# Kernel optimization log

Measured on AMD Instinct MI355X. Metric: run time of the kernel, lower is better.

## Reference

```python
import math
import jax, jax.numpy as jnp
import numpy as np

CHUNK = 32
EPS = 1e-5


def l2norm(x):
    return x * jax.lax.rsqrt(jnp.sum(x * x, -1, keepdims=True))


def causal_dwconv(x, w):
    # x: (B, C, L); w: (C, K) depthwise causal conv (left pad K-1)
    C, K = w.shape
    return jax.lax.conv_general_dilated(x, w[:, None, :], (1,), [(K - 1, 0)], feature_group_count=C)


def per_head_stats(x):
    # x: (B,L,H,D) -> (B,L,H,4): mean, var(pop), abs-mean, l2-norm
    mean = jnp.mean(x, -1, keepdims=True)
    var = jnp.mean(x * x, -1, keepdims=True) - mean * mean
    abs_mean = jnp.mean(jnp.abs(x), -1, keepdims=True)
    l2 = jnp.sqrt(jnp.sum(x * x, -1, keepdims=True))
    return jnp.concatenate([mean, var, abs_mean, l2], -1)


def delta_rule_chunkwise(q, k, v, beta, chunk=CHUNK):
    # q,k: (B,H,L,dk); v: (B,H,L,dv); beta: (B,H,L)
    b, h, L, dk = q.shape
    dv = v.shape[-1]
    pad = (-L) % chunk
    if pad:
        pc = ((0, 0), (0, 0), (0, pad), (0, 0))
        q, k, v = (jnp.pad(t, pc) for t in (q, k, v))
        beta = jnp.pad(beta, ((0, 0), (0, 0), (0, pad)))
    Lp = L + pad
    n = Lp // chunk
    q = l2norm(q)
    k = l2norm(k)
    v = v * beta[..., None]
    kb = k * beta[..., None]
    resh = lambda t: t.reshape(b, h, n, chunk, t.shape[-1])
    q, k, v, kb = map(resh, (q, k, v, kb))
    tri = jnp.triu(jnp.ones((chunk, chunk), bool))          # incl. diag
    strict = jnp.triu(jnp.ones((chunk, chunk), bool), 1)    # above diag
    A = jnp.where(tri, 0.0, -jnp.einsum('bhncd,bhned->bhnce', kb, k))
    # forward-substitution inverse of (I - strict_lower) as in the torch loop
    for i in range(1, chunk):
        upd = jnp.einsum('...k,...kj->...j', A[..., i, :], A[..., :, :i])
        A = A.at[..., i, :i].add(upd)
    inv = A + jnp.eye(chunk, dtype=A.dtype)
    u = inv @ v   # (b,h,n,c,dv)
    w = inv @ kb  # (b,h,n,c,dk)

    def step(S, xs):
        qi, ki, ui, wi = xs  # (b,h,c,d)
        attn = jnp.where(strict, 0.0, qi @ jnp.swapaxes(ki, -1, -2))
        u_adj = ui - wi @ S
        out_i = qi @ S + attn @ u_adj
        S = S + jnp.swapaxes(ki, -1, -2) @ u_adj
        return S, out_i

    xs = tuple(jnp.moveaxis(t, 2, 0) for t in (q, k, u, w))
    S0 = jnp.zeros((b, h, dk, dv), q.dtype)
    S, outs = jax.lax.scan(step, S0, xs)
    out = jnp.moveaxis(outs, 0, 2).reshape(b, h, Lp, dv)[:, :, :L]
    return out, S


def reference(hidden_states, q_proj_w, k_proj_w, v_proj_w, b_proj_w,
              q_conv_w, k_conv_w, v_conv_w, fir_short_w, fir_long_w,
              fuse_w1, fuse_b1, fuse_w2, fuse_b2, logit_temp,
              res_scale_short, res_scale_long, o_norm_w, o_proj_w):
    B, L, D = hidden_states.shape
    H = fir_short_w.shape[0]

    def shortconv(x, w):  # x: (B,L,C)
        y = causal_dwconv(jnp.swapaxes(x, 1, 2), w)
        return jax.nn.silu(jnp.swapaxes(y, 1, 2))

    q = shortconv(hidden_states @ q_proj_w.T, q_conv_w)
    k = shortconv(hidden_states @ k_proj_w.T, k_conv_w)
    v = shortconv(hidden_states @ v_proj_w.T, v_conv_w)
    q = q.reshape(B, L, H, -1)
    k = k.reshape(B, L, H, -1)
    v_direct = v.reshape(B, L, H, -1)
    beta = jax.nn.sigmoid(hidden_states @ b_proj_w.T)  # (B,L,H)

    delta_out, _S = delta_rule_chunkwise(
        jnp.transpose(q, (0, 2, 1, 3)), jnp.transpose(k, (0, 2, 1, 3)),
        jnp.transpose(v_direct, (0, 2, 1, 3)), jnp.transpose(beta, (0, 2, 1)))
    delta_out = jnp.transpose(delta_out, (0, 2, 1, 3))

    def fir(x, filt):  # x: (B,L,H,Dh); filt: (H,Dh,K)
        hh, dd, kk = filt.shape
        xf = jnp.swapaxes(x.reshape(B, L, hh * dd), 1, 2)
        y = causal_dwconv(xf, filt.reshape(hh * dd, kk))
        return jnp.swapaxes(y, 1, 2).reshape(B, L, hh, dd)

    local_short = fir(v_direct, fir_short_w)
    local_long = fir(v_direct, fir_long_w)

    stats = jnp.concatenate([per_head_stats(t) for t in
                             (local_short, local_long, delta_out, v_direct)], -1)  # (B,L,H,16)
    hs_exp = jnp.broadcast_to(hidden_states[:, :, None, :], (B, L, H, D))
    gate_in = jnp.concatenate([hs_exp, stats], -1)
    hdn = jax.nn.gelu(gate_in @ fuse_w1.T + fuse_b1, approximate=False)
    logits = hdn @ fuse_w2.T + fuse_b2  # (B,L,H,4)
    temp = jax.nn.softplus(logit_temp) + 1e-4
    fw = jax.nn.softmax(logits / temp, -1)

    o = (fw[..., 0:1] * local_short + fw[..., 1:2] * local_long
         + fw[..., 2:3] * delta_out + fw[..., 3:4] * v_direct)
    o = o + res_scale_short * local_short + res_scale_long * local_long
    o = o * jax.lax.rsqrt(jnp.mean(o * o, -1, keepdims=True) + EPS) * o_norm_w
    return o.reshape(B, L, -1) @ o_proj_w.T


def setup_inputs() -> dict:
    key = jax.random.key(0)
    ks = jax.random.split(key, 16)
    B, L, D, H = 2, 4096, 1024, 4
    dk, dv = D, D
    dh = dv // H
    gate_in_dim = D + 16
    gate_hidden = D * 2 // 2
    s = 0.02
    f32 = jnp.float32
    return {
        'hidden_states': jax.random.normal(ks[0], (B, L, D), f32),
        'q_proj_w': jax.random.normal(ks[1], (dk, D), f32) * s,
        'k_proj_w': jax.random.normal(ks[2], (dk, D), f32) * s,
        'v_proj_w': jax.random.normal(ks[3], (dv, D), f32) * s,
        'b_proj_w': jax.random.normal(ks[4], (H, D), f32) * s,
        'q_conv_w': jax.random.normal(ks[5], (dk, 4), f32) * 0.1,
        'k_conv_w': jax.random.normal(ks[6], (dk, 4), f32) * 0.1,
        'v_conv_w': jax.random.normal(ks[7], (dv, 4), f32) * 0.1,
        'fir_short_w': jax.random.normal(ks[8], (H, dh, 5), f32) * 0.02,
        'fir_long_w': jax.random.normal(ks[9], (H, dh, 64), f32) * 0.02,
        'fuse_w1': jax.random.normal(ks[10], (gate_hidden, gate_in_dim), f32) * s,
        'fuse_b1': jnp.zeros((gate_hidden,), f32),
        'fuse_w2': jax.random.normal(ks[11], (4, gate_hidden), f32) * s,
        'fuse_b2': jnp.array([-1.0, -1.0, 1.0, 3.0], f32),
        'logit_temp': jnp.full((1,), math.log(math.expm1(0.7)), f32),
        'res_scale_short': jnp.full((1,), 0.1, f32),
        'res_scale_long': jnp.full((1,), 0.1, f32),
        'o_norm_w': jnp.ones((dh,), f32),
        'o_proj_w': jax.random.normal(ks[12], (D, dv), f32) * s,
    }
```

## Files before the change

kernel.cpp:

```cpp
#include <hip/hip_runtime.h>
#include <hip/hip_bf16.h>

#define BB 2
#define LL 4096
#define DD 1024
#define HH 4
#define DH 256
#define CH 32
#define NC (LL/CH)
#define BL (BB*LL)
#define BLD ((size_t)BB*LL*DD)

typedef __attribute__((ext_vector_type(8))) short short8;
typedef __attribute__((ext_vector_type(4))) float floatx4;

__device__ __forceinline__ float bf2f(unsigned short u) {
    union { float f; unsigned int i; } x; x.i = ((unsigned int)u) << 16; return x.f;
}
__device__ __forceinline__ float bflo(unsigned int u) {
    union { float f; unsigned int i; } x; x.i = u << 16; return x.f;
}
__device__ __forceinline__ float bfhi(unsigned int u) {
    union { float f; unsigned int i; } x; x.i = u & 0xFFFF0000u; return x.f;
}
__device__ __forceinline__ unsigned short f2bf(float f) {
    union { float f; unsigned int i; } x; x.f = f;
    unsigned int r = x.i + 0x7FFFu + ((x.i >> 16) & 1u);
    return (unsigned short)(r >> 16);
}
__device__ __forceinline__ unsigned int pkbf(float a, float b) {
    unsigned int ua = __float_as_uint(a) + 0x8000u;
    unsigned int ub = __float_as_uint(b) + 0x8000u;
    return __builtin_amdgcn_perm(ub, ua, 0x07060302);
}
__device__ __forceinline__ void lds_barrier() {
    __builtin_amdgcn_s_waitcnt(0xC07F);
    __builtin_amdgcn_s_barrier();
}
__device__ __forceinline__ short8 gload16(const void* p) {
    short8 r;
    asm volatile("global_load_dwordx4 %0, %1, off" : "=v"(r) : "v"(p) : "memory");
    return r;
}
__device__ __forceinline__ uint2 gload8(const void* p) {
    uint2 r;
    asm volatile("global_load_dwordx2 %0, %1, off" : "=v"(r) : "v"(p) : "memory");
    return r;
}

__global__ __launch_bounds__(256) void cvt_bf_k(
    const float* __restrict__ x, unsigned short* __restrict__ y)
{
    size_t i = ((size_t)blockIdx.x * 256 + threadIdx.x) * 4;
    float4 v = *(const float4*)(x + i);
    ushort4 o;
    o.x = f2bf(v.x); o.y = f2bf(v.y); o.z = f2bf(v.z); o.w = f2bf(v.w);
    *(ushort4*)(y + i) = o;
}

__global__ __launch_bounds__(256) void w1s_prep_k(
    const float* __restrict__ w1, unsigned short* __restrict__ w1s)
{
    int idx = blockIdx.x * 256 + threadIdx.x;
    int e = idx >> 4, s = idx & 15;
    w1s[idx] = f2bf(w1[(size_t)e * 1040 + 1024 + s]);
}

__global__ __launch_bounds__(256) void gemm_mfma(
    const float* __restrict__ A, int lda,
    const float* __restrict__ W, int ldw,
    const float* __restrict__ bias,
    float* __restrict__ C, int ldc, int K)
{
    __shared__ unsigned short Abuf[128][56];
    __shared__ unsigned short Bbuf[128][56];
    const int t = threadIdx.x;
    const int wave = t >> 6, lane = t & 63;
    const int wm = wave >> 1, wn = wave & 1;
    const int row0 = blockIdx.y * 128, col0 = blockIdx.x * 128;

    floatx4 acc[4][4];
#pragma unroll
    for (int i = 0; i < 4; ++i)
#pragma unroll
        for (int j = 0; j < 4; ++j) acc[i][j] = (floatx4){0.f, 0.f, 0.f, 0.f};

    const int fr = lane & 15, fk = (lane >> 4) * 8;

    for (int kt = 0; kt < K; kt += 32) {
        __syncthreads();
#pragma unroll
        for (int it = 0; it < 2; ++it) {
            int idx = t + it * 256;
            int r = idx >> 2, s = (idx & 3) * 8;
            const float* ap = A + (size_t)(row0 + r) * lda + kt + s;
            float4 a0 = *(const float4*)(ap);
            float4 a1 = *(const float4*)(ap + 4);
            ushort4 p0, p1;
            p0.x = f2bf(a0.x); p0.y = f2bf(a0.y); p0.z = f2bf(a0.z); p0.w = f2bf(a0.w);
            p1.x = f2bf(a1.x); p1.y = f2bf(a1.y); p1.z = f2bf(a1.z); p1.w = f2bf(a1.w);
            *(ushort4*)&Abuf[r][s]     = p0;
            *(ushort4*)&Abuf[r][s + 4] = p1;
            const float* wp = W + (size_t)(col0 + r) * ldw + kt + s;
            float4 b0 = *(const float4*)(wp);
            float4 b1 = *(const float4*)(wp + 4);
            ushort4 q0, q1;
            q0.x = f2bf(b0.x); q0.y = f2bf(b0.y); q0.z = f2bf(b0.z); q0.w = f2bf(b0.w);
            q1.x = f2bf(b1.x); q1.y = f2bf(b1.y); q1.z = f2bf(b1.z); q1.w = f2bf(b1.w);
            *(ushort4*)&Bbuf[r][s]     = q0;
            *(ushort4*)&Bbuf[r][s + 4] = q1;
        }
        __syncthreads();

        short8 afrag[4], bfrag[4];
#pragma unroll
        for (int i = 0; i < 4; ++i) {
            afrag[i] = *(const short8*)&Abuf[wm * 64 + i * 16 + fr][fk];
            bfrag[i] = *(const short8*)&Bbuf[wn * 64 + i * 16 + fr][fk];
        }
#pragma unroll
        for (int i = 0; i < 4; ++i)
#pragma unroll
            for (int j = 0; j < 4; ++j)
                acc[i][j] = __builtin_amdgcn_mfma_f32_16x16x32_bf16(
                    afrag[i], bfrag[j], acc[i][j], 0, 0, 0);
    }

    const int fc = lane & 15, frow = (lane >> 4) * 4;
#pragma unroll
    for (int j = 0; j < 4; ++j) {
        int col = col0 + wn * 64 + j * 16 + fc;
        float bv = bias ? bias[col] : 0.0f;
#pragma unroll
        for (int i = 0; i < 4; ++i) {
#pragma unroll
            for (int r = 0; r < 4; ++r) {
                int row = row0 + wm * 64 + i * 16 + frow + r;
                C[(size_t)row * ldc + col] = acc[i][j][r] + bv;
            }
        }
    }
}

__global__ __launch_bounds__(256) void gemm_bb(
    const unsigned short* __restrict__ A, int lda,
    const unsigned short* __restrict__ B, int ldb,
    float* __restrict__ C, int ldc, int K)
{
    __shared__ unsigned short Abuf[128][56];
    __shared__ unsigned short Bbuf[128][56];
    const int t = threadIdx.x;
    const int wave = t >> 6, lane = t & 63;
    const int wm = wave >> 1, wn = wave & 1;
    const int row0 = blockIdx.y * 128, col0 = blockIdx.x * 128;

    floatx4 acc[4][4];
#pragma unroll
    for (int i = 0; i < 4; ++i)
#pragma unroll
        for (int j = 0; j < 4; ++j) acc[i][j] = (floatx4){0.f, 0.f, 0.f, 0.f};

    const int fr = lane & 15, fk = (lane >> 4) * 8;

    for (int kt = 0; kt < K; kt += 32) {
        __syncthreads();
#pragma unroll
        for (int it = 0; it < 2; ++it) {
            int idx = t + it * 256;
            int r = idx >> 2, s = (idx & 3) * 8;
            uint4 av = *(const uint4*)(A + (size_t)(row0 + r) * lda + kt + s);
            *(uint4*)&Abuf[r][s] = av;
            uint4 bv = *(const uint4*)(B + (size_t)(col0 + r) * ldb + kt + s);
            *(uint4*)&Bbuf[r][s] = bv;
        }
        __syncthreads();

        short8 afrag[4], bfrag[4];
#pragma unroll
        for (int i = 0; i < 4; ++i) {
            afrag[i] = *(const short8*)&Abuf[wm * 64 + i * 16 + fr][fk];
            bfrag[i] = *(const short8*)&Bbuf[wn * 64 + i * 16 + fr][fk];
        }
#pragma unroll
        for (int i = 0; i < 4; ++i)
#pragma unroll
            for (int j = 0; j < 4; ++j)
                acc[i][j] = __builtin_amdgcn_mfma_f32_16x16x32_bf16(
                    afrag[i], bfrag[j], acc[i][j], 0, 0, 0);
    }

    const int fc = lane & 15, frow = (lane >> 4) * 4;
#pragma unroll
    for (int j = 0; j < 4; ++j) {
        int col = col0 + wn * 64 + j * 16 + fc;
#pragma unroll
        for (int i = 0; i < 4; ++i) {
#pragma unroll
            for (int r = 0; r < 4; ++r) {
                int row = row0 + wm * 64 + i * 16 + frow + r;
                C[(size_t)row * ldc + col] = acc[i][j][r];
            }
        }
    }
}

__global__ __launch_bounds__(256) void convnorm_qk_k(
    const float* __restrict__ x, const float* __restrict__ w,
    unsigned short* __restrict__ y)
{
    int bl = blockIdx.x >> 2;
    int h  = blockIdx.x & 3;
    int l  = bl & (LL - 1);
    int d  = threadIdx.x;
    int c  = h * DH + d;
    const float* wp = w + (size_t)c * 4;
    const float* xp = x + (size_t)bl * DD + c;
    float acc = wp[3] * xp[0];
    if (l >= 1) acc += wp[2] * xp[-(int)DD];
    if (l >= 2) acc += wp[1] * xp[-2*(int)DD];
    if (l >= 3) acc += wp[0] * xp[-3*(int)DD];
    acc = acc / (1.0f + expf(-acc));
    float s = acc * acc;
#pragma unroll
    for (int off = 32; off > 0; off >>= 1) s += __shfl_down(s, off);
    __shared__ float red[4];
    int wv = threadIdx.x >> 6, ln = threadIdx.x & 63;
    if (ln == 0) red[wv] = s;
    __syncthreads();
    float tot = red[0] + red[1] + red[2] + red[3];
    y[(size_t)bl * DD + c] = f2bf(acc * rsqrtf(tot));
}

__global__ __launch_bounds__(256) void conv_silu_k(
    const float* __restrict__ x, const float* __restrict__ w, float* __restrict__ y)
{
    size_t idx = (size_t)blockIdx.x * 256 + threadIdx.x;
    int c = (int)(idx & (DD - 1));
    int bl = (int)(idx >> 10);
    int l = bl & (LL - 1);
    const float* wp = w + (size_t)c * 4;
    const float* xp = x + (size_t)bl * DD + c;
    float acc = wp[3] * xp[0];
    if (l >= 1) acc += wp[2] * xp[-(int)DD];
    if (l >= 2) acc += wp[1] * xp[-2*(int)DD];
    if (l >= 3) acc += wp[0] * xp[-3*(int)DD];
    y[idx] = acc / (1.0f + expf(-acc));
}

template<int K>
__global__ __launch_bounds__(256) void fir2_k(
    const float* __restrict__ x, const float* __restrict__ filt, float* __restrict__ y)
{
    const int ctile = blockIdx.x & 15;
    const int ltile = (blockIdx.x >> 4) & 63;
    const int b = blockIdx.x >> 10;
    const int RT = 64 + K - 1;
    __shared__ float xs[RT][64];
    __shared__ float fs[64][K + 1];
    const int t = threadIdx.x;
    const int l0 = ltile * 64;

    for (int i = t; i < RT * 16; i += 256) {
        int li = i >> 4, c4 = (i & 15) * 4;
        int l = l0 - (K - 1) + li;
        float4 v = make_float4(0.f, 0.f, 0.f, 0.f);
        if (l >= 0)
            v = *(const float4*)(x + ((size_t)b * LL + l) * DD + ctile * 64 + c4);
        *(float4*)&xs[li][c4] = v;
    }
    for (int i = t; i < 64 * K; i += 256) {
        fs[i / K][i % K] = filt[(size_t)ctile * 64 * K + i];
    }
    __syncthreads();

    const int c = t & 63, lg = t >> 6;
    float acc[16];
#pragma unroll
    for (int o = 0; o < 16; ++o) acc[o] = 0.f;
#pragma unroll
    for (int j = 0; j < 16 + K - 1; ++j) {
        float xv = xs[lg * 16 + j][c];
#pragma unroll
        for (int o = 0; o < 16; ++o) {
            int tap = j - o;
            if (tap >= 0 && tap < K) acc[o] += fs[c][tap] * xv;
        }
    }
    size_t base = ((size_t)b * LL + l0 + lg * 16) * DD + ctile * 64 + c;
#pragma unroll
    for (int o = 0; o < 16; ++o)
        y[base + (size_t)o * DD] = acc[o];
}

__global__ __launch_bounds__(256) void beta_k(
    const float* __restrict__ hs, const float* __restrict__ bw, float* __restrict__ beta)
{
    int bl = blockIdx.x;
    const float* xr = hs + (size_t)bl * DD;
    float a0=0.f,a1=0.f,a2=0.f,a3=0.f;
    for (int k = threadIdx.x; k < DD; k += 256) {
        float xv = xr[k];
        a0 += xv * bw[k];
        a1 += xv * bw[DD + k];
        a2 += xv * bw[2*DD + k];
        a3 += xv * bw[3*DD + k];
    }
#pragma unroll
    for (int off = 32; off > 0; off >>= 1) {
        a0 += __shfl_down(a0, off); a1 += __shfl_down(a1, off);
        a2 += __shfl_down(a2, off); a3 += __shfl_down(a3, off);
    }
    __shared__ float red[4][4];
    int wv = threadIdx.x >> 6, ln = threadIdx.x & 63;
    if (ln == 0) { red[wv][0]=a0; red[wv][1]=a1; red[wv][2]=a2; red[wv][3]=a3; }
    __syncthreads();
    if (threadIdx.x < 4) {
        int h = threadIdx.x;
        float s = red[0][h] + red[1][h] + red[2][h] + red[3][h];
        beta[(size_t)bl * HH + h] = 1.0f / (1.0f + expf(-s));
    }
}

__global__ __launch_bounds__(256) void tr_k(
    const unsigned short* __restrict__ k, unsigned short* __restrict__ kT)
{
    int et = blockIdx.x & 3;
    int lt = (blockIdx.x >> 2) & 63;
    int bh = blockIdx.x >> 8;
    int h = bh & 3, b = bh >> 2;
    __shared__ unsigned short tile[64][72];
    int t = threadIdx.x;
    int tr = t >> 4;
    int tc = (t & 15) * 4;
#pragma unroll
    for (int i = 0; i < 4; ++i) {
        int l = tr + i * 16;
        ushort4 v = *(const ushort4*)(k + ((size_t)b * LL + lt*64 + l) * DD + h * DH + et*64 + tc);
        *(ushort4*)&tile[l][tc] = v;
    }
    __syncthreads();
#pragma unroll
    for (int i = 0; i < 4; ++i) {
        int e = tr + i * 16;
        ushort4 v;
        v.x = tile[tc+0][e]; v.y = tile[tc+1][e];
        v.z = tile[tc+2][e]; v.w = tile[tc+3][e];
        *(ushort4*)(kT + ((size_t)bh * DH + et*64 + e) * LL + (size_t)lt*64 + tc) = v;
    }
}

__global__ __launch_bounds__(256) void chunk_prep2_k(
    const unsigned short* __restrict__ q, const unsigned short* __restrict__ k,
    const unsigned short* __restrict__ kT, const float* __restrict__ v,
    const float* __restrict__ beta,
    unsigned short* __restrict__ uT, unsigned short* __restrict__ w_out,
    unsigned short* __restrict__ attn_out)
{
    const int ci = blockIdx.x & (NC - 1);
    const int bh = blockIdx.x >> 7;
    const int h = bh & (HH - 1), b = bh >> 2;
    __shared__ unsigned short kL[32][264];
    __shared__ unsigned short qL[32][264];
    __shared__ float vL[32][260];
    __shared__ float AmL[32][33];
    __shared__ unsigned short AbH[32][40];
    __shared__ unsigned short AbL2[32][40];
    __shared__ float betL[32];
    const int t = threadIdx.x;
    const int wave = t >> 6, lane = t & 63;
    const int lr = lane & 15, lg = lane >> 4;
    const int l0 = ci * CH;
    const size_t rowbase = (size_t)b * LL + l0;

    for (int i = t; i < 1024; i += 256) {
        int r = i >> 5, s8 = (i & 31) * 8;
        *(uint4*)&kL[r][s8] = *(const uint4*)(k + (rowbase + r) * DD + h * DH + s8);
        *(uint4*)&qL[r][s8] = *(const uint4*)(q + (rowbase + r) * DD + h * DH + s8);
    }
    for (int i = t; i < 2048; i += 256) {
        int e = i >> 6, d4 = (i & 63) * 4;
        *(float4*)&vL[e][d4] = *(const float4*)(v + (rowbase + e) * DD + h * DH + d4);
    }
    if (t < 32) betL[t] = beta[(rowbase + t) * HH + h];
    __syncthreads();

    const int mt = wave >> 1, nt = wave & 1;
    floatx4 accA = (floatx4){0.f,0.f,0.f,0.f}, accT = accA;
#pragma unroll
    for (int ks = 0; ks < 8; ++ks) {
        short8 bk = *(const short8*)&kL[nt * 16 + lr][ks * 32 + lg * 8];
        short8 ak = *(const short8*)&kL[mt * 16 + lr][ks * 32 + lg * 8];
        short8 aq = *(const short8*)&qL[mt * 16 + lr][ks * 32 + lg * 8];
        accA = __builtin_amdgcn_mfma_f32_16x16x32_bf16(ak, bk, accA, 0, 0, 0);
        accT = __builtin_amdgcn_mfma_f32_16x16x32_bf16(aq, bk, accT, 0, 0, 0);
    }
    {
        const size_t abase = (size_t)blockIdx.x * (CH * CH);
        const int ee = nt * 16 + lr;
#pragma unroll
        for (int r = 0; r < 4; ++r) {
            int c = mt * 16 + lg * 4 + r;
            float bc = betL[c];
            AmL[c][ee] = (ee < c) ? (-bc * accA[r]) : 0.0f;
            attn_out[abase + (size_t)c * CH + ee] =
                (ee <= c) ? f2bf(accT[r]) : (unsigned short)0;
        }
    }
    __syncthreads();

    const unsigned short* kTg = kT + (size_t)bh * DH * LL;
    short8 wB[4];
#pragma unroll
    for (int n = 0; n < 4; ++n)
        wB[n] = *(const short8*)(kTg + (size_t)(wave * 64 + n * 16 + lr) * LL + l0 + lg * 8);

    if (wave == 0) {
        const int j = lane & 31;
        float col[32];
#pragma unroll
        for (int c = 0; c < 32; ++c) col[c] = AmL[c][j];
#pragma unroll
        for (int i = 1; i < 32; ++i) {
            float u0 = 0.f, u1 = 0.f;
#pragma unroll
            for (int kk = 0; kk < 32; kk += 2) {
                if (kk < i)     u0 += __shfl(col[i], kk) * col[kk];
                if (kk + 1 < i) u1 += __shfl(col[i], kk + 1) * col[kk + 1];
            }
            if (j < i) col[i] += u0 + u1;
        }
        if (lane < 32) {
            const float bj = betL[j];
#pragma unroll
            for (int c = 0; c < 32; ++c) {
                float val = (col[c] + (c == j ? 1.0f : 0.0f)) * bj;
                unsigned short hi = f2bf(val);
                AbH[c][j] = hi;
                AbL2[c][j] = f2bf(val - bf2f(hi));
            }
        }
    }
    __syncthreads();

    short8 AH[2], ALo[2];
#pragma unroll
    for (int m = 0; m < 2; ++m) {
        AH[m]  = *(const short8*)&AbH[m * 16 + lr][lg * 8];
        ALo[m] = *(const short8*)&AbL2[m * 16 + lr][lg * 8];
    }
    const size_t uTbase = (size_t)bh * DH * LL;
    const size_t wbase  = (size_t)bh * LL * DH;
#pragma unroll
    for (int n = 0; n < 4; ++n) {
        const int d = wave * 64 + n * 16 + lr;
        union { short8 s8; unsigned int u[4]; } vf;
#pragma unroll
        for (int p2 = 0; p2 < 4; ++p2)
            vf.u[p2] = pkbf(vL[lg * 8 + p2 * 2][d], vL[lg * 8 + p2 * 2 + 1][d]);
#pragma unroll
        for (int m = 0; m < 2; ++m) {
            floatx4 au = (floatx4){0.f,0.f,0.f,0.f};
            au = __builtin_amdgcn_mfma_f32_16x16x32_bf16(AH[m],  vf.s8, au, 0, 0, 0);
            au = __builtin_amdgcn_mfma_f32_16x16x32_bf16(ALo[m], vf.s8, au, 0, 0, 0);
            ushort4 ou;
            ou.x = f2bf(au[0]); ou.y = f2bf(au[1]); ou.z = f2bf(au[2]); ou.w = f2bf(au[3]);
            *(ushort4*)(uT + uTbase + (size_t)d * LL + l0 + m * 16 + lg * 4) = ou;

            floatx4 aw = (floatx4){0.f,0.f,0.f,0.f};
            aw = __builtin_amdgcn_mfma_f32_16x16x32_bf16(AH[m],  wB[n], aw, 0, 0, 0);
            aw = __builtin_amdgcn_mfma_f32_16x16x32_bf16(ALo[m], wB[n], aw, 0, 0, 0);
#pragma unroll
            for (int r = 0; r < 4; ++r)
                w_out[wbase + (size_t)(l0 + m * 16 + lg * 4 + r) * DH + d] = f2bf(aw[r]);
        }
    }
}

__global__ __launch_bounds__(256, 1) void scan12_k(
    const unsigned short* __restrict__ q, const unsigned short* __restrict__ kT,
    const unsigned short* __restrict__ uT, const unsigned short* __restrict__ w,
    const unsigned short* __restrict__ attn, float* __restrict__ dout)
{
    const int bh = blockIdx.x & 7;
    const int jb = blockIdx.x >> 3;
    const int h = bh & (HH - 1), b = bh >> 2;
    const int jcol = jb * 16;
    const int wave = threadIdx.x >> 6, lane = threadIdx.x & 63;
    const int lr = lane & 15, lg = lane >> 4;
    const int half = wave & 1;
    const bool isQ = wave >= 2;

    __shared__ unsigned short SbT[16][264];
    __shared__ unsigned short uadjT[16][40];

    floatx4 Sacc[4];
#pragma unroll
    for (int mt = 0; mt < 4; ++mt) Sacc[mt] = (floatx4){0.f,0.f,0.f,0.f};

    const unsigned short* qb  = q + (size_t)b * LL * DD + h * DH;
    const unsigned short* wb  = w + (size_t)bh * LL * DH;
    const unsigned short* ob  = isQ ? qb : wb;
    const size_t ost          = isQ ? (size_t)DD : (size_t)DH;
    const unsigned short* orow0 = ob + (size_t)(half * 16 + lr) * ost + lg * 8;
    const unsigned short* kTb = kT + (size_t)bh * DH * LL
                                + (size_t)(64 * wave + lr) * LL + lg * 8;
    const unsigned short* uTb = uT + ((size_t)bh * DH + jcol + lr) * LL + half * 16 + lg * 4;
    const unsigned short* atb = attn + (size_t)bh * NC * (CH * CH)
                                + (size_t)(half * 16 + lr) * CH + lg * 8;
    float* db = dout + (size_t)bh * LL * DH;

    short8 po[2][8];
    short8 pk[2][4];
    short8 pa[2];
    uint2  pu[2];

#define ISSUE13(cn, s)                                                          \
    {                                                                           \
        const int ln_ = (cn) * CH;                                              \
        const unsigned short* orow_ = orow0 + (size_t)ln_ * ost;                \
        po[s][0] = gload16(orow_ + 0*32);  po[s][1] = gload16(orow_ + 1*32);    \
        po[s][2] = gload16(orow_ + 2*32);  po[s][3] = gload16(orow_ + 3*32);    \
        po[s][4] = gload16(orow_ + 4*32);  po[s][5] = gload16(orow_ + 5*32);    \
        po[s][6] = gload16(orow_ + 6*32);  po[s][7] = gload16(orow_ + 7*32);    \
        pk[s][0] = gload16(kTb + (size_t)(0*16) * LL + ln_);                    \
        pk[s][1] = gload16(kTb + (size_t)(1*16) * LL + ln_);                    \
        pk[s][2] = gload16(kTb + (size_t)(2*16) * LL + ln_);                    \
        pk[s][3] = gload16(kTb + (size_t)(3*16) * LL + ln_);                    \
        if (!isQ) pu[s] = gload8(uTb + ln_);                                    \
        else      pa[s] = gload16(atb + (size_t)(cn) * (CH * CH));              \
    }

    ISSUE13(0, 0);

#pragma unroll 2
    for (int ci = 0; ci < NC; ++ci) {
        const int p = ci & 1;
        const int l0 = ci * CH;

        {
            const int cn = (ci + 1 < NC) ? (ci + 1) : ci;
            ISSUE13(cn, p ^ 1);
        }

#pragma unroll
        for (int mt = 0; mt < 4; ++mt) {
            int e0 = 64 * wave + 16 * mt + lg * 4;
            *(uint2*)&SbT[lr][e0] = make_uint2(pkbf(Sacc[mt][0], Sacc[mt][1]),
                                               pkbf(Sacc[mt][2], Sacc[mt][3]));
        }
        lds_barrier();

        if (!isQ || ci == 0) { asm volatile("s_waitcnt vmcnt(13)" ::: "memory"); }
        else                 { asm volatile("s_waitcnt vmcnt(17)" ::: "memory"); }
        __builtin_amdgcn_sched_barrier(0);

        floatx4 Pa = (floatx4){0.f,0.f,0.f,0.f}, Pb = Pa;
#pragma unroll
        for (int kt = 0; kt < 4; ++kt) {
            short8 s0 = *(const short8*)&SbT[lr][(2*kt)   * 32 + lg * 8];
            short8 s1 = *(const short8*)&SbT[lr][(2*kt+1) * 32 + lg * 8];
            Pa = __builtin_amdgcn_mfma_f32_16x16x32_bf16(po[p][2*kt],   s0, Pa, 0,0,0);
            Pb = __builtin_amdgcn_mfma_f32_16x16x32_bf16(po[p][2*kt+1], s1, Pb, 0,0,0);
        }
        floatx4 P = Pa + Pb;

        if (!isQ) {
            float ua0 = bflo(pu[p].x) - P[0];
            float ua1 = bfhi(pu[p].x) - P[1];
            float ua2 = bflo(pu[p].y) - P[2];
            float ua3 = bfhi(pu[p].y) - P[3];
            int cc0 = half * 16 + lg * 4;
            *(uint2*)&uadjT[lr][cc0] = make_uint2(pkbf(ua0, ua1), pkbf(ua2, ua3));
        }
        lds_barrier();

        short8 ub = *(const short8*)&uadjT[lr][lg * 8];

        if (isQ) {
            floatx4 Ot = __builtin_amdgcn_mfma_f32_16x16x32_bf16(pa[p], ub, P, 0,0,0);
#pragma unroll
            for (int r = 0; r < 4; ++r)
                db[(size_t)(l0 + half * 16 + lg * 4 + r) * DH + jcol + lr] = Ot[r];
        }

#pragma unroll
        for (int mt = 0; mt < 4; ++mt)
            Sacc[mt] = __builtin_amdgcn_mfma_f32_16x16x32_bf16(pk[p][mt], ub, Sacc[mt], 0,0,0);
    }
#undef ISSUE13
}

__global__ __launch_bounds__(256) void stats_k(
    const float* __restrict__ ls, const float* __restrict__ llb,
    const float* __restrict__ dox, const float* __restrict__ v,
    float* __restrict__ stats)
{
    int bl = blockIdx.x;
    int b = bl >> 12, l = bl & (LL - 1);
    int wv = threadIdx.x >> 6, ln = threadIdx.x & 63;
    size_t ibase = (size_t)bl * DD + wv * DH;
    size_t dbase = (((size_t)(b * HH + wv)) * LL + l) * DH;
#pragma unroll
    for (int tn = 0; tn < 4; ++tn) {
        const float* p; size_t base;
        if (tn == 0)      { p = ls;  base = ibase; }
        else if (tn == 1) { p = llb; base = ibase; }
        else if (tn == 2) { p = dox; base = dbase; }
        else              { p = v;   base = ibase; }
        float4 x = *(const float4*)(p + base + ln * 4);
        float sm = x.x + x.y + x.z + x.w;
        float sq = x.x*x.x + x.y*x.y + x.z*x.z + x.w*x.w;
        float sa = fabsf(x.x) + fabsf(x.y) + fabsf(x.z) + fabsf(x.w);
#pragma unroll
        for (int off = 32; off > 0; off >>= 1) {
            sm += __shfl_down(sm, off);
            sq += __shfl_down(sq, off);
            sa += __shfl_down(sa, off);
        }
        if (ln == 0) {
            float mean = sm * (1.0f / DH);
            float var = sq * (1.0f / DH) - mean * mean;
            float am = sa * (1.0f / DH);
            float l2 = sqrtf(sq);
            *(float4*)(stats + (size_t)bl * 64 + wv * 16 + tn * 4) =
                make_float4(mean, var, am, l2);
        }
    }
}

__global__ __launch_bounds__(256) void gate_fin2_k(
    const float* __restrict__ hpart, const float* __restrict__ stats,
    const unsigned short* __restrict__ w1s,
    const float* __restrict__ w2, const float* __restrict__ b2,
    const float* __restrict__ ltemp, float* __restrict__ fw)
{
    const int bl = blockIdx.x;
    const int t = threadIdx.x;
    const float temp = log1pf(expf(ltemp[0])) + 1e-4f;
    __shared__ float st[HH][16];
    __shared__ float red[4][16];
    __shared__ float fin[16];
    if (t < 64) st[t >> 4][t & 15] = stats[(size_t)bl * 64 + t];

    const int e0 = t * 4;
    float4 hp4 = *(const float4*)(hpart + (size_t)bl * DD + e0);
    float hp[4] = {hp4.x, hp4.y, hp4.z, hp4.w};
    float w2a[4][4];
#pragma unroll
    for (int j = 0; j < 4; ++j) {
        float4 wv = *(const float4*)(w2 + (size_t)j * 1024 + e0);
        w2a[j][0] = wv.x; w2a[j][1] = wv.y; w2a[j][2] = wv.z; w2a[j][3] = wv.w;
    }
    uint4 wpk[8];
    const uint4* wp = (const uint4*)(w1s + (size_t)e0 * 16);
#pragma unroll
    for (int i = 0; i < 8; ++i) wpk[i] = wp[i];
    __syncthreads();

    float lg[4][4];
#pragma unroll
    for (int h = 0; h < 4; ++h)
#pragma unroll
        for (int j = 0; j < 4; ++j) lg[h][j] = 0.0f;

#pragma unroll
    for (int ii = 0; ii < 4; ++ii) {
        float xh[4] = {hp[ii], hp[ii], hp[ii], hp[ii]};
        unsigned arr[8] = {wpk[ii*2].x, wpk[ii*2].y, wpk[ii*2].z, wpk[ii*2].w,
                           wpk[ii*2+1].x, wpk[ii*2+1].y, wpk[ii*2+1].z, wpk[ii*2+1].w};
#pragma unroll
        for (int p = 0; p < 8; ++p) {
            float wlo = bflo(arr[p]), whi = bfhi(arr[p]);
            int s = p * 2;
#pragma unroll
            for (int h = 0; h < 4; ++h)
                xh[h] += st[h][s] * wlo + st[h][s + 1] * whi;
        }
#pragma unroll
        for (int h = 0; h < 4; ++h) {
            float x = xh[h];
            float gct = 0.5f * x * (1.0f + erff(x * 0.70710678118654752f));
            lg[h][0] += gct * w2a[0][ii];
            lg[h][1] += gct * w2a[1][ii];
            lg[h][2] += gct * w2a[2][ii];
            lg[h][3] += gct * w2a[3][ii];
        }
    }

#pragma unroll
    for (int h = 0; h < 4; ++h)
#pragma unroll
        for (int j = 0; j < 4; ++j)
#pragma unroll
            for (int off = 32; off > 0; off >>= 1)
                lg[h][j] += __shfl_down(lg[h][j], off);

    const int wv = t >> 6, ln = t & 63;
    if (ln == 0) {
#pragma unroll
        for (int h = 0; h < 4; ++h)
#pragma unroll
            for (int j = 0; j < 4; ++j) red[wv][h * 4 + j] = lg[h][j];
    }
    __syncthreads();
    if (t < 16) {
        float s = red[0][t] + red[1][t] + red[2][t] + red[3][t] + b2[t & 3];
        fin[t] = s / temp;
    }
    __syncthreads();
    if (t < 4) {
        float l0 = fin[t*4], l1 = fin[t*4+1], l2 = fin[t*4+2], l3 = fin[t*4+3];
        float m = fmaxf(fmaxf(l0, l1), fmaxf(l2, l3));
        float e0x = expf(l0-m), e1 = expf(l1-m), e2 = expf(l2-m), e3 = expf(l3-m);
        float inv = 1.0f / (e0x + e1 + e2 + e3);
        *(float4*)(fw + (size_t)bl * 16 + t * 4) = make_float4(e0x*inv, e1*inv, e2*inv, e3*inv);
    }
}

__global__ __launch_bounds__(256) void combine_k(
    const float* __restrict__ ls, const float* __restrict__ llb,
    const float* __restrict__ dox, const float* __restrict__ v,
    const float* __restrict__ fw, const float* __restrict__ rss,
    const float* __restrict__ rsl, const float* __restrict__ onw,
    float* __restrict__ opre)
{
    int h = blockIdx.x & (HH - 1);
    int bl = blockIdx.x >> 2;
    int b = bl >> 12, l = bl & (LL - 1);
    int d = threadIdx.x;
    size_t i1 = (size_t)blockIdx.x * DH + d;
    size_t i2 = (((size_t)(b * HH + h)) * LL + l) * DH + d;
    const float* fwp = fw + (size_t)blockIdx.x * 4;
    float f0 = fwp[0], f1 = fwp[1], f2 = fwp[2], f3 = fwp[3];
    float aS = rss[0], aL = rsl[0];
    float vls = ls[i1], vll = llb[i1], vd = dox[i2], vv = v[i1];
    float o = f0*vls + f1*vll + f2*vd + f3*vv + aS*vls + aL*vll;
    float s = o * o;
#pragma unroll
    for (int off = 32; off > 0; off >>= 1) s += __shfl_down(s, off);
    __shared__ float red[4];
    int wv = threadIdx.x >> 6, ln = threadIdx.x & 63;
    if (ln == 0) red[wv] = s;
    __syncthreads();
    float ms = (red[0] + red[1] + red[2] + red[3]) * (1.0f / DH);
    opre[(size_t)bl * DD + h * DH + d] = o * rsqrtf(ms + 1e-5f) * onw[d];
}

extern "C" void kernel_launch(void* const* d_in, const int* in_sizes, int n_in,
                              void* d_out, int out_size, void* d_ws, size_t ws_size,
                              hipStream_t stream)
{
    const float* hs  = (const float*)d_in[0];
    const float* qw  = (const float*)d_in[1];
    const float* kw  = (const float*)d_in[2];
    const float* vw  = (const float*)d_in[3];
    const float* bw  = (const float*)d_in[4];
    const float* qcw = (const float*)d_in[5];
    const float* kcw = (const float*)d_in[6];
    const float* vcw = (const float*)d_in[7];
    const float* fsw = (const float*)d_in[8];
    const float* flw = (const float*)d_in[9];
    const float* w1  = (const float*)d_in[10];
    const float* b1  = (const float*)d_in[11];
    const float* w2  = (const float*)d_in[12];
    const float* b2  = (const float*)d_in[13];
    const float* lt  = (const float*)d_in[14];
    const float* rss = (const float*)d_in[15];
    const float* rsl = (const float*)d_in[16];
    const float* onw = (const float*)d_in[17];
    const float* opw = (const float*)d_in[18];
    float* out = (float*)d_out;

    float* wsf = (float*)d_ws;
    float* tmp   = wsf;
    unsigned short* ktbuf = (unsigned short*)tmp;
    unsigned short* uTbuf = (unsigned short*)(wsf + BLD/2);
    float* vbuf  = wsf + BLD;
    float* dbuf  = wsf + 2*BLD;
    unsigned short* hsb = (unsigned short*)(wsf + 2*BLD);
    unsigned short* qwb = (unsigned short*)(wsf + 2*BLD + BLD/2);
    unsigned short* kwb = qwb + (size_t)DD*DD;
    unsigned short* vwb = kwb + (size_t)DD*DD;
    unsigned short* qbuf = (unsigned short*)(wsf + 3*BLD);
    unsigned short* kbuf = qbuf + BLD;
    float* hpart = wsf + 3*BLD;
    float* opre  = wsf + 3*BLD;
    unsigned short* ubuf = (unsigned short*)(wsf + 4*BLD);
    unsigned short* wbuf = ubuf + BLD;
    float* llbuf = wsf + 4*BLD;
    float* lsbuf = tmp;
    unsigned short* attnb = (unsigned short*)(wsf + 5*BLD);
    float* statsb = wsf + 5*BLD + 524288;
    float* fwbuf  = statsb + (size_t)BL*HH*16;
    float* betab  = fwbuf + (size_t)BL*HH*4;
    unsigned short* w1sp = (unsigned short*)(betab + (size_t)BL*HH);

    dim3 gg(8, 64);

    cvt_bf_k<<<(int)(BLD/1024), 256, 0, stream>>>(hs, hsb);
    cvt_bf_k<<<1024, 256, 0, stream>>>(qw, qwb);
    cvt_bf_k<<<1024, 256, 0, stream>>>(kw, kwb);
    cvt_bf_k<<<1024, 256, 0, stream>>>(vw, vwb);
    w1s_prep_k<<<64, 256, 0, stream>>>(w1, w1sp);

    gemm_bb<<<gg, 256, 0, stream>>>(hsb, DD, qwb, DD, tmp, DD, DD);
    convnorm_qk_k<<<BL*HH, 256, 0, stream>>>(tmp, qcw, qbuf);
    gemm_bb<<<gg, 256, 0, stream>>>(hsb, DD, kwb, DD, tmp, DD, DD);
    convnorm_qk_k<<<BL*HH, 256, 0, stream>>>(tmp, kcw, kbuf);
    gemm_bb<<<gg, 256, 0, stream>>>(hsb, DD, vwb, DD, tmp, DD, DD);
    conv_silu_k<<<(int)(BLD/256), 256, 0, stream>>>(tmp, vcw, vbuf);

    beta_k<<<BL, 256, 0, stream>>>(hs, bw, betab);

    tr_k<<<8*64*4, 256, 0, stream>>>(kbuf, ktbuf);
    chunk_prep2_k<<<BB*HH*NC, 256, 0, stream>>>(qbuf, kbuf, ktbuf, vbuf, betab,
                                                uTbuf, wbuf, attnb);

    scan12_k<<<BB*HH*16, 256, 0, stream>>>(qbuf, ktbuf, uTbuf, wbuf, attnb, dbuf);

    fir2_k<5><<<BB*64*16, 256, 0, stream>>>(vbuf, fsw, lsbuf);
    fir2_k<64><<<BB*64*16, 256, 0, stream>>>(vbuf, flw, llbuf);

    stats_k<<<BL, 256, 0, stream>>>(lsbuf, llbuf, dbuf, vbuf, statsb);

    gemm_mfma<<<gg, 256, 0, stream>>>(hs, DD, w1, 1040, b1, hpart, DD, DD);
    gate_fin2_k<<<BL, 256, 0, stream>>>(hpart, statsb, w1sp, w2, b2, lt, fwbuf);

    combine_k<<<BL*HH, 256, 0, stream>>>(lsbuf, llbuf, dbuf, vbuf, fwbuf, rss, rsl, onw, opre);

    gemm_mfma<<<gg, 256, 0, stream>>>(opre, DD, opw, DD, nullptr, out, DD, DD);
}
```

Before: 886.1 us.

## Pre-swizzle q/kT/w/uT into per-chunk fragment layout, drop transpose kernel

Removes the separate k transpose kernel. The chunk prep kernel now writes q, k-transposed, w and u-transposed in a per-chunk MFMA-fragment-tiled layout, building the k transpose from the k tile already held in LDS. The serial scan kernel can then load each operand fragment as a contiguous 16-byte read instead of strided row accesses. The cost is an extra copy of q written by prep and byte-scattered w stores, in exchange for one fewer launch and more coalesced loads in the latency-bound scan.

```diff
diff --git a/kernel.cpp b/kernel.cpp
--- a/kernel.cpp
+++ b/kernel.cpp
@@ -321,39 +321,11 @@
     }
 }
 
-__global__ __launch_bounds__(256) void tr_k(
-    const unsigned short* __restrict__ k, unsigned short* __restrict__ kT)
-{
-    int et = blockIdx.x & 3;
-    int lt = (blockIdx.x >> 2) & 63;
-    int bh = blockIdx.x >> 8;
-    int h = bh & 3, b = bh >> 2;
-    __shared__ unsigned short tile[64][72];
-    int t = threadIdx.x;
-    int tr = t >> 4;
-    int tc = (t & 15) * 4;
-#pragma unroll
-    for (int i = 0; i < 4; ++i) {
-        int l = tr + i * 16;
-        ushort4 v = *(const ushort4*)(k + ((size_t)b * LL + lt*64 + l) * DD + h * DH + et*64 + tc);
-        *(ushort4*)&tile[l][tc] = v;
-    }
-    __syncthreads();
-#pragma unroll
-    for (int i = 0; i < 4; ++i) {
-        int e = tr + i * 16;
-        ushort4 v;
-        v.x = tile[tc+0][e]; v.y = tile[tc+1][e];
-        v.z = tile[tc+2][e]; v.w = tile[tc+3][e];
-        *(ushort4*)(kT + ((size_t)bh * DH + et*64 + e) * LL + (size_t)lt*64 + tc) = v;
-    }
-}
-
-__global__ __launch_bounds__(256) void chunk_prep2_k(
+__global__ __launch_bounds__(256) void chunk_prep3_k(
     const unsigned short* __restrict__ q, const unsigned short* __restrict__ k,
-    const unsigned short* __restrict__ kT, const float* __restrict__ v,
-    const float* __restrict__ beta,
-    unsigned short* __restrict__ uT, unsigned short* __restrict__ w_out,
+    const float* __restrict__ v, const float* __restrict__ beta,
+    unsigned short* __restrict__ qt, unsigned short* __restrict__ kTt,
+    unsigned short* __restrict__ wt, unsigned short* __restrict__ uTt,
     unsigned short* __restrict__ attn_out)
 {
     const int ci = blockIdx.x & (NC - 1);
@@ -408,12 +380,8 @@
     }
     __syncthreads();
 
-    const unsigned short* kTg = kT + (size_t)bh * DH * LL;
-    short8 wB[4];
-#pragma unroll
-    for (int n = 0; n < 4; ++n)
-        wB[n] = *(const short8*)(kTg + (size_t)(wave * 64 + n * 16 + lr) * LL + l0 + lg * 8);
-
+    unsigned short* qtc  = qt  + (size_t)blockIdx.x * 8192;
+    unsigned short* kTtc = kTt + (size_t)blockIdx.x * 8192;
     if (wave == 0) {
         const int j = lane & 31;
         float col[32];
@@ -439,6 +407,22 @@
                 AbL2[c][j] = f2bf(val - bf2f(hi));
             }
         }
+    } else {
+        for (int o = t - 64; o < 2048; o += 192) {
+            if (o < 1024) {
+                int lg2 = o & 3, lr2 = (o >> 2) & 15, kt2 = (o >> 6) & 7, hf = o >> 9;
+                short8 val = *(const short8*)&qL[hf * 16 + lr2][kt2 * 32 + lg2 * 8];
+                *(short8*)(qtc + (size_t)o * 8) = val;
+            } else {
+                int o2 = o - 1024;
+                int lg2 = o2 & 3, lr2 = (o2 >> 2) & 15, mt2 = (o2 >> 6) & 3, wv = o2 >> 8;
+                int e = wv * 64 + mt2 * 16 + lr2;
+                union { short8 s8; unsigned short u[8]; } val;
+#pragma unroll
+                for (int j2 = 0; j2 < 8; ++j2) val.u[j2] = kL[lg2 * 8 + j2][e];
+                *(short8*)(kTtc + (size_t)o2 * 8) = val.s8;
+            }
+        }
     }
     __syncthreads();
 
@@ -448,8 +432,7 @@
         AH[m]  = *(const short8*)&AbH[m * 16 + lr][lg * 8];
         ALo[m] = *(const short8*)&AbL2[m * 16 + lr][lg * 8];
     }
-    const size_t uTbase = (size_t)bh * DH * LL;
-    const size_t wbase  = (size_t)bh * LL * DH;
+    unsigned short* wtc = wt + (size_t)blockIdx.x * 8192;
 #pragma unroll
     for (int n = 0; n < 4; ++n) {
         const int d = wave * 64 + n * 16 + lr;
@@ -457,6 +440,12 @@
 #pragma unroll
         for (int p2 = 0; p2 < 4; ++p2)
             vf.u[p2] = pkbf(vL[lg * 8 + p2 * 2][d], vL[lg * 8 + p2 * 2 + 1][d]);
+        union { short8 s8; unsigned short u[8]; } wBv;
+#pragma unroll
+        for (int j2 = 0; j2 < 8; ++j2) wBv.u[j2] = kL[lg * 8 + j2][d];
+
+        const int jb2 = wave * 4 + n;
+        unsigned short* utc = uTt + ((size_t)(bh * 16 + jb2) * NC + ci) * 512;
 #pragma unroll
         for (int m = 0; m < 2; ++m) {
             floatx4 au = (floatx4){0.f,0.f,0.f,0.f};
@@ -464,26 +453,28 @@
             au = __builtin_amdgcn_mfma_f32_16x16x32_bf16(ALo[m], vf.s8, au, 0, 0, 0);
             ushort4 ou;
             ou.x = f2bf(au[0]); ou.y = f2bf(au[1]); ou.z = f2bf(au[2]); ou.w = f2bf(au[3]);
-            *(ushort4*)(uT + uTbase + (size_t)d * LL + l0 + m * 16 + lg * 4) = ou;
+            *(ushort4*)(utc + m * 256 + lr * 16 + lg * 4) = ou;
 
             floatx4 aw = (floatx4){0.f,0.f,0.f,0.f};
-            aw = __builtin_amdgcn_mfma_f32_16x16x32_bf16(AH[m],  wB[n], aw, 0, 0, 0);
-            aw = __builtin_amdgcn_mfma_f32_16x16x32_bf16(ALo[m], wB[n], aw, 0, 0, 0);
-#pragma unroll
-            for (int r = 0; r < 4; ++r)
-                w_out[wbase + (size_t)(l0 + m * 16 + lg * 4 + r) * DH + d] = f2bf(aw[r]);
-        }
-    }
-}
-
-__global__ __launch_bounds__(256, 1) void scan12_k(
-    const unsigned short* __restrict__ q, const unsigned short* __restrict__ kT,
-    const unsigned short* __restrict__ uT, const unsigned short* __restrict__ w,
+            aw = __builtin_amdgcn_mfma_f32_16x16x32_bf16(AH[m],  wBv.s8, aw, 0, 0, 0);
+            aw = __builtin_amdgcn_mfma_f32_16x16x32_bf16(ALo[m], wBv.s8, aw, 0, 0, 0);
+#pragma unroll
+            for (int r = 0; r < 4; ++r) {
+                int off = m * 4096 + (d >> 5) * 512 + (lg * 4 + r) * 32
+                          + ((d >> 3) & 3) * 8 + (d & 7);
+                wtc[off] = f2bf(aw[r]);
+            }
+        }
+    }
+}
+
+__global__ __launch_bounds__(256, 1) void scan13_k(
+    const unsigned short* __restrict__ qt, const unsigned short* __restrict__ kTt,
+    const unsigned short* __restrict__ uTt, const unsigned short* __restrict__ wt,
     const unsigned short* __restrict__ attn, float* __restrict__ dout)
 {
     const int bh = blockIdx.x & 7;
     const int jb = blockIdx.x >> 3;
-    const int h = bh & (HH - 1), b = bh >> 2;
     const int jcol = jb * 16;
     const int wave = threadIdx.x >> 6, lane = threadIdx.x & 63;
     const int lr = lane & 15, lg = lane >> 4;
@@ -495,18 +486,16 @@
 
     floatx4 Sacc[4];
 #pragma unroll
-    for (int mt = 0; mt < 4; ++mt) Sacc[mt] = (floatx4){0.f,0.f,0.f,0.f};
-
-    const unsigned short* qb  = q + (size_t)b * LL * DD + h * DH;
-    const unsigned short* wb  = w + (size_t)bh * LL * DH;
-    const unsigned short* ob  = isQ ? qb : wb;
-    const size_t ost          = isQ ? (size_t)DD : (size_t)DH;
-    const unsigned short* orow0 = ob + (size_t)(half * 16 + lr) * ost + lg * 8;
-    const unsigned short* kTb = kT + (size_t)bh * DH * LL
-                                + (size_t)(64 * wave + lr) * LL + lg * 8;
-    const unsigned short* uTb = uT + ((size_t)bh * DH + jcol + lr) * LL + half * 16 + lg * 4;
-    const unsigned short* atb = attn + (size_t)bh * NC * (CH * CH)
-                                + (size_t)(half * 16 + lr) * CH + lg * 8;
+    for (int mtv = 0; mtv < 4; ++mtv) Sacc[mtv] = (floatx4){0.f,0.f,0.f,0.f};
+
+    const unsigned short* potb = (isQ ? qt : wt) + (size_t)bh * NC * 8192
+                                 + half * 4096 + lr * 32 + lg * 8;
+    const unsigned short* kttb = kTt + (size_t)bh * NC * 8192
+                                 + wave * 2048 + lr * 32 + lg * 8;
+    const unsigned short* uttb = uTt + (size_t)(bh * 16 + jb) * NC * 512
+                                 + half * 256 + lr * 16 + lg * 4;
+    const unsigned short* atb  = attn + (size_t)bh * NC * 1024
+                                 + (half * 16 + lr) * 32 + lg * 8;
     float* db = dout + (size_t)bh * LL * DH;
 
     short8 po[2][8];
@@ -516,18 +505,21 @@
 
 #define ISSUE13(cn, s)                                                          \
     {                                                                           \
-        const int ln_ = (cn) * CH;                                              \
-        const unsigned short* orow_ = orow0 + (size_t)ln_ * ost;                \
-        po[s][0] = gload16(orow_ + 0*32);  po[s][1] = gload16(orow_ + 1*32);    \
-        po[s][2] = gload16(orow_ + 2*32);  po[s][3] = gload16(orow_ + 3*32);    \
-        po[s][4] = gload16(orow_ + 4*32);  po[s][5] = gload16(orow_ + 5*32);    \
-        po[s][6] = gload16(orow_ + 6*32);  po[s][7] = gload16(orow_ + 7*32);    \
-        pk[s][0] = gload16(kTb + (size_t)(0*16) * LL + ln_);                    \
-        pk[s][1] = gload16(kTb + (size_t)(1*16) * LL + ln_);                    \
-        pk[s][2] = gload16(kTb + (size_t)(2*16) * LL + ln_);                    \
-        pk[s][3] = gload16(kTb + (size_t)(3*16) * LL + ln_);                    \
-        if (!isQ) pu[s] = gload8(uTb + ln_);                                    \
-        else      pa[s] = gload16(atb + (size_t)(cn) * (CH * CH));              \
+        const size_t co_ = (size_t)(cn) * 8192;                                 \
+        po[s][0] = gload16(potb + co_ + 0*512);                                 \
+        po[s][1] = gload16(potb + co_ + 1*512);                                 \
+        po[s][2] = gload16(potb + co_ + 2*512);                                 \
+        po[s][3] = gload16(potb + co_ + 3*512);                                 \
+        po[s][4] = gload16(potb + co_ + 4*512);                                 \
+        po[s][5] = gload16(potb + co_ + 5*512);                                 \
+        po[s][6] = gload16(potb + co_ + 6*512);                                 \
+        po[s][7] = gload16(potb + co_ + 7*512);                                 \
+        pk[s][0] = gload16(kttb + co_ + 0*512);                                 \
+        pk[s][1] = gload16(kttb + co_ + 1*512);                                 \
+        pk[s][2] = gload16(kttb + co_ + 2*512);                                 \
+        pk[s][3] = gload16(kttb + co_ + 3*512);                                 \
+        if (!isQ) pu[s] = gload8(uttb + (size_t)(cn) * 512);                    \
+        else      pa[s] = gload16(atb + (size_t)(cn) * 1024);                   \
     }
 
     ISSUE13(0, 0);
@@ -543,10 +535,10 @@
         }
 
 #pragma unroll
-        for (int mt = 0; mt < 4; ++mt) {
-            int e0 = 64 * wave + 16 * mt + lg * 4;
-            *(uint2*)&SbT[lr][e0] = make_uint2(pkbf(Sacc[mt][0], Sacc[mt][1]),
-                                               pkbf(Sacc[mt][2], Sacc[mt][3]));
+        for (int mtv = 0; mtv < 4; ++mtv) {
+            int e0 = 64 * wave + 16 * mtv + lg * 4;
+            *(uint2*)&SbT[lr][e0] = make_uint2(pkbf(Sacc[mtv][0], Sacc[mtv][1]),
+                                               pkbf(Sacc[mtv][2], Sacc[mtv][3]));
         }
         lds_barrier();
 
@@ -584,8 +576,8 @@
         }
 
 #pragma unroll
-        for (int mt = 0; mt < 4; ++mt)
-            Sacc[mt] = __builtin_amdgcn_mfma_f32_16x16x32_bf16(pk[p][mt], ub, Sacc[mt], 0,0,0);
+        for (int mtv = 0; mtv < 4; ++mtv)
+            Sacc[mtv] = __builtin_amdgcn_mfma_f32_16x16x32_bf16(pk[p][mtv], ub, Sacc[mtv], 0,0,0);
     }
 #undef ISSUE13
 }
@@ -773,8 +765,8 @@
 
     float* wsf = (float*)d_ws;
     float* tmp   = wsf;
-    unsigned short* ktbuf = (unsigned short*)tmp;
-    unsigned short* uTbuf = (unsigned short*)(wsf + BLD/2);
+    unsigned short* kTtb = (unsigned short*)tmp;
+    unsigned short* uTtb = (unsigned short*)(wsf + BLD/2);
     float* vbuf  = wsf + BLD;
     float* dbuf  = wsf + 2*BLD;
     unsigned short* hsb = (unsigned short*)(wsf + 2*BLD);
@@ -785,8 +777,8 @@
     unsigned short* kbuf = qbuf + BLD;
     float* hpart = wsf + 3*BLD;
     float* opre  = wsf + 3*BLD;
-    unsigned short* ubuf = (unsigned short*)(wsf + 4*BLD);
-    unsigned short* wbuf = ubuf + BLD;
+    unsigned short* qtb = (unsigned short*)(wsf + 4*BLD);
+    unsigned short* wtb = qtb + BLD;
     float* llbuf = wsf + 4*BLD;
     float* lsbuf = tmp;
     unsigned short* attnb = (unsigned short*)(wsf + 5*BLD);
@@ -812,11 +804,10 @@
 
     beta_k<<<BL, 256, 0, stream>>>(hs, bw, betab);
 
-    tr_k<<<8*64*4, 256, 0, stream>>>(kbuf, ktbuf);
-    chunk_prep2_k<<<BB*HH*NC, 256, 0, stream>>>(qbuf, kbuf, ktbuf, vbuf, betab,
-                                                uTbuf, wbuf, attnb);
-
-    scan12_k<<<BB*HH*16, 256, 0, stream>>>(qbuf, ktbuf, uTbuf, wbuf, attnb, dbuf);
+    chunk_prep3_k<<<BB*HH*NC, 256, 0, stream>>>(qbuf, kbuf, vbuf, betab,
+                                                qtb, kTtb, wtb, uTtb, attnb);
+
+    scan13_k<<<BB*HH*16, 256, 0, stream>>>(qtb, kTtb, uTtb, wtb, attnb, dbuf);
 
     fir2_k<5><<<BB*64*16, 256, 0, stream>>>(vbuf, fsw, lsbuf);
     fir2_k<64><<<BB*64*16, 256, 0, stream>>>(vbuf, flw, llbuf);
```

Result: faster. 807.3 us (-8.9%).
